# Kernel tuning notes

Measured on AMD Instinct MI355X. Metric: run time of the kernel, lower is better.

The kernel has to match this reference:

```python
import jax, jax.numpy as jnp
import numpy as np

EMB = 128
EA = 32
ET = 32
NN = 50000
NE = 320000
NBAND = 3
LAM = 0.01  # softshrink sparsity_threshold
LN_EPS = 1e-5


def _softshrink(x, lam=LAM):
    return jnp.where(x > lam, x - lam, jnp.where(x < -lam, x + lam, jnp.zeros_like(x)))


def _forward(hidden, edge_attr, edge_time_emb, boundary_condition,
             alpha, r1, i1, rb1, ib1, fre_w, fre_b,
             comb_w, comb_b, lin_w, lin_b, ln_g, ln_b, edge_index):
    num_nodes = hidden.shape[0]
    # gather source node features and concat edge features -> [E, d_in]
    x = jnp.concatenate([hidden[edge_index[0]], edge_attr, edge_time_emb], axis=1)
    # FreMLP: FFT over feature dim (real input -> complex64)
    x_fft = jnp.fft.fft(x)
    xr, xi = x_fft.real, x_fft.imag
    energy = jnp.sum(xr * xr + xi * xi, axis=-1)  # [E]
    energy_sum = jnp.sum(energy)
    outs = []
    for k in range(NBAND):
        factor = (2.0 * (k + 1) - 1.0) / (2.0 * NBAND)
        Qk = alpha[k] * factor * energy_sum
        bk = energy_sum / (alpha[k] * (2.0 * NBAND))
        mask = ((energy >= Qk - bk) & (energy <= Qk + bk)).astype(x.dtype)[:, None]
        fr = xr * mask
        fi = xi * mask
        # complex linear: (fr + i*fi) @ (r1 + i*i1) + (rb1 + i*ib1)
        o_r = fr @ r1[k] - fi @ i1[k] + rb1[k]
        o_i = fi @ r1[k] + fr @ i1[k] + ib1[k]
        o_r = _softshrink(jax.nn.relu(o_r))
        o_i = _softshrink(jax.nn.relu(o_i))
        outs.append(jax.lax.complex(o_r, o_i))
    y_fft = jnp.concatenate(outs, axis=-1)  # [E, NBAND*EMB] complex
    y = jnp.fft.ifft(y_fft).real
    msg = y @ fre_w + fre_b  # [E, EMB]
    # view_as_complex(msg, 0) -> view_as_real -> flatten: interleave real with zeros
    msg_ri = jnp.stack([msg, jnp.zeros_like(msg)], axis=-1).reshape(msg.shape[0], 2 * EMB)
    msg2 = msg_ri @ comb_w + comb_b  # [E, EMB]
    # scatter-reduce(sum) into destination nodes + boundary self-loops
    msg_aug = jnp.concatenate([msg2, boundary_condition], axis=0)
    idx_aug = jnp.concatenate([edge_index[1], jnp.arange(num_nodes, dtype=edge_index.dtype)])
    out = jax.ops.segment_sum(msg_aug, idx_aug, num_segments=num_nodes)
    out = out @ lin_w + lin_b
    mu = jnp.mean(out, axis=-1, keepdims=True)
    var = jnp.mean((out - mu) ** 2, axis=-1, keepdims=True)
    out = (out - mu) * jax.lax.rsqrt(var + LN_EPS) * ln_g + ln_b
    return jax.nn.relu(out)  # dropout is identity in eval mode


def setup_inputs() -> dict:
    key = jax.random.key(0)
    ks = jax.random.split(key, 16)
    d_in = EMB + EA + ET
    s = 0.02
    return {
        "hidden": jax.random.normal(ks[0], (NN, EMB), jnp.float32),
        "edge_attr": jax.random.normal(ks[1], (NE, EA), jnp.float32),
        "edge_time_emb": jax.random.normal(ks[2], (NE, ET), jnp.float32),
        "boundary_condition": jax.random.normal(ks[3], (NN, EMB), jnp.float32),
        "alpha": jnp.ones((NBAND,), jnp.float32),
        "r1": s * jax.random.normal(ks[4], (NBAND, d_in, EMB), jnp.float32),
        "i1": s * jax.random.normal(ks[5], (NBAND, d_in, EMB), jnp.float32),
        "rb1": s * jax.random.normal(ks[6], (NBAND, EMB), jnp.float32),
        "ib1": s * jax.random.normal(ks[7], (NBAND, EMB), jnp.float32),
        "fre_w": s * jax.random.normal(ks[8], (NBAND * EMB, EMB), jnp.float32),
        "fre_b": s * jax.random.normal(ks[9], (EMB,), jnp.float32),
        "comb_w": s * jax.random.normal(ks[10], (2 * EMB, EMB), jnp.float32),
        "comb_b": s * jax.random.normal(ks[11], (EMB,), jnp.float32),
        "lin_w": s * jax.random.normal(ks[12], (EMB, EMB), jnp.float32),
        "lin_b": s * jax.random.normal(ks[13], (EMB,), jnp.float32),
        "ln_g": jnp.ones((EMB,), jnp.float32),
        "ln_b": jnp.zeros((EMB,), jnp.float32),
        "edge_index": jax.random.randint(ks[14], (2, NE), 0, NN, dtype=jnp.int32),
    }


def reference(hidden, edge_attr, edge_time_emb, boundary_condition, alpha, r1, i1, rb1, ib1,
              fre_w, fre_b, comb_w, comb_b, lin_w, lin_b, ln_g, ln_b, edge_index):
    return _forward(hidden, edge_attr, edge_time_emb, boundary_condition, alpha, r1, i1,
                    rb1, ib1, fre_w, fre_b, comb_w, comb_b, lin_w, lin_b, ln_g, ln_b, edge_index)
```

## Files before the change

### kernel.cpp

```cpp
#include <hip/hip_runtime.h>
#include <hip/hip_bf16.h>

#define NNODES 50000
#define NEDGES 320000
#define EMB 128
#define DIN 192
#define NB 3
#define LAM 0.01f
#define LN_EPS 1e-5f
#define PI_F 3.14159265358979323846f

#define SCAN_B 196
#define SCAN_N (SCAN_B * 256)

typedef __attribute__((ext_vector_type(8))) short v8s;
typedef __attribute__((ext_vector_type(4))) float v4f;
typedef __attribute__((ext_vector_type(2))) float v2f;

#define WS_ESUM 0
#define WS_WB   16
#define WS_G2B  (WS_WB + 73728)
#define WS_G2   (WS_G2B + 49152)
#define WS_PHI  (WS_G2 + 98304)
#define WS_M    (WS_PHI + 98304)
#define WS_BB   (WS_M + 16384)
#define WS_GB2  (WS_BB + 768)
#define WS_CK   (WS_GB2 + 128)
#define WS_EN   (WS_CK + 384)
#define WS_NORM (WS_EN + NEDGES)
#define WS_CNT  (WS_NORM + NNODES)
#define WS_CUR  (WS_CNT + SCAN_N)
#define WS_PART (WS_CUR + SCAN_N)
#define WS_EIDS (WS_PART + 256)

__device__ __forceinline__ unsigned pk2(float a, float b) {
  __hip_bfloat162 h2 = __float22bfloat162_rn(make_float2(a, b));
  return *reinterpret_cast<unsigned*>(&h2);
}

__device__ __forceinline__ void atomic2(float* dp, float a, float b) {
#if __has_builtin(__builtin_amdgcn_flat_atomic_fadd_v2f32)
  v2f val; val.x = a; val.y = b;
  __builtin_amdgcn_flat_atomic_fadd_v2f32((v2f*)dp, val);
#else
  atomicAdd(dp, a); atomicAdd(dp + 1, b);
#endif
}

__global__ __launch_bounds__(256) void k_prep1(
    const float* __restrict__ r1, const float* __restrict__ i1,
    __hip_bfloat16* __restrict__ Wb, const float* __restrict__ comb_w,
    const float* __restrict__ lin_w, float* __restrict__ M,
    const float* __restrict__ fre_w, float* __restrict__ Phi,
    const float* __restrict__ hidden, float* __restrict__ norms) {
  __shared__ float cs[384], sn[384];
  const int t = threadIdx.x;
  const int b = blockIdx.x;
  if (b < 576) {
    if (t < 192) sincosf((2.f * PI_F / 192.f) * (float)t, &sn[t], &cs[t]);
    __syncthreads();
    int idx = b * 256 + t;
    int n = idx / 768, c = idx - (idx / 768) * 768;
    int k = c >> 8, col = c & 255;
    int isI = col >> 7, j = col & 127;
    const float* ap = (isI ? i1 : r1) + (size_t)k * DIN * EMB + j;
    const float* bp = (isI ? r1 : i1) + (size_t)k * DIN * EMB + j;
    float sgn = isI ? -1.f : 1.f;
    float acc = 0.f;
    int m = 0;
    for (int f = 0; f < DIN; ++f) {
      acc = fmaf(cs[m], ap[(size_t)f * EMB], fmaf(sgn * sn[m], bp[(size_t)f * EMB], acc));
      m += n; if (m >= 192) m -= 192;
    }
    int kc = n >> 5, quad = (n & 31) >> 3, jj = n & 7;
    int lane = quad * 16 + (col & 15);
    Wb[((((k * 6 + kc) * 16 + (col >> 4)) * 64) + lane) * 8 + jj] = __float2bfloat16(acc);
  } else if (b < 640) {
    int idx = (b - 576) * 256 + t;
    int j = idx >> 7, j2 = idx & 127;
    float acc = 0.f;
    for (int tt = 0; tt < 128; ++tt)
      acc = fmaf(comb_w[(2 * j) * 128 + tt], lin_w[tt * 128 + j2], acc);
    M[idx] = acc;
  } else if (b < 1024) {
    for (int i = t; i < 384; i += 256)
      sincosf((2.f * PI_F / 384.f) * (float)i, &sn[i], &cs[i]);
    __syncthreads();
    int idx = (b - 640) * 256 + t;
    int slot = idx >> 7, j1 = idx & 127;
    int k = slot >> 8, r = slot & 255;
    int isI = r >> 7;
    int f = k * 128 + (r & 127);
    const float* tp = isI ? sn : cs;
    float sg = isI ? -1.f : 1.f;
    float acc = 0.f;
    int m = 0;
    for (int n = 0; n < 384; ++n) {
      acc = fmaf(sg * tp[m], fre_w[n * 128 + j1], acc);
      m += f; if (m >= 384) m -= 384;
    }
    Phi[slot * 128 + j1] = acc * (1.f / 384.f);
  } else {
    const int w = t >> 6, lane = t & 63;
    const int n = (b - 1024) * 4 + w;
    const float2 v = ((const float2*)(hidden + (size_t)n * 128))[lane];
    float ss = v.x * v.x + v.y * v.y;
#pragma unroll
    for (int off = 32; off > 0; off >>= 1) ss += __shfl_xor(ss, off, 64);
    if (lane == 0) norms[n] = ss;
  }
}

__global__ __launch_bounds__(256) void k_prep2(
    const float* __restrict__ Phi, const float* __restrict__ M,
    float* __restrict__ G2, __hip_bfloat16* __restrict__ G2b,
    const float* __restrict__ norms, const float* __restrict__ eattr,
    const float* __restrict__ ett, const int* __restrict__ eidx,
    float* __restrict__ energies, float* __restrict__ esum,
    int* __restrict__ cnt) {
  const int t = threadIdx.x;
  const int b = blockIdx.x;
  if (b < 384) {
    int idx = b * 256 + t;
    int slot = idx >> 7, j2 = idx & 127;
    float acc = 0.f;
    for (int j1 = 0; j1 < 128; ++j1)
      acc = fmaf(Phi[slot * 128 + j1], M[j1 * 128 + j2], acc);
    G2[idx] = acc;
    int k = slot >> 8, s = slot & 255;
    int kc = s >> 5, quad = (s & 31) >> 3, jj = s & 7;
    G2b[((((k * 8 + kc) * 8 + (j2 >> 4)) * 64) + quad * 16 + (j2 & 15)) * 8 + jj] =
        __float2bfloat16(acc);
  } else {
    int e = (b - 384) * 256 + t;
    float ss = norms[eidx[e]];
    const float4* a4 = (const float4*)(eattr + (size_t)e * 32);
#pragma unroll
    for (int i = 0; i < 8; ++i) {
      float4 v = a4[i];
      ss += v.x * v.x + v.y * v.y + v.z * v.z + v.w * v.w;
    }
    const float4* t4 = (const float4*)(ett + (size_t)e * 32);
#pragma unroll
    for (int i = 0; i < 8; ++i) {
      float4 v = t4[i];
      ss += v.x * v.x + v.y * v.y + v.z * v.z + v.w * v.w;
    }
    float en = 192.f * ss;
    energies[e] = en;
    float tot = en;
#pragma unroll
    for (int off = 32; off > 0; off >>= 1) tot += __shfl_down(tot, off, 64);
    if ((t & 63) == 0) atomicAdd(esum, tot);
    atomicAdd(&cnt[eidx[NEDGES + e]], 1);
  }
}

__global__ __launch_bounds__(256) void k_prep3(
    const float* __restrict__ rb1, const float* __restrict__ ib1,
    const float* __restrict__ fre_b, const float* __restrict__ comb_b,
    const float* __restrict__ lin_w, const float* __restrict__ M,
    const float* __restrict__ G2, float* __restrict__ bb,
    float* __restrict__ gb2, float* __restrict__ ck,
    int* __restrict__ cnt, int* __restrict__ part) {
  __shared__ int sm[256];
  const int t = threadIdx.x;
  const int b = blockIdx.x;
  if (b < 5) {
    int idx = b * 256 + t;
    if (idx < 768) {
      int k = idx >> 8, r = idx & 255;
      bb[idx] = (r >= 128) ? ib1[k * 128 + (r & 127)] : rb1[k * 128 + r];
    } else if (idx < 896) {
      int j2 = idx - 768;
      float acc = 0.f;
      for (int j = 0; j < 128; ++j) acc += fre_b[j] * M[j * 128 + j2];
      for (int tt = 0; tt < 128; ++tt) acc += comb_b[tt] * lin_w[tt * 128 + j2];
      gb2[j2] = acc;
    } else if (idx < 1280) {
      int q = idx - 896;
      int k = q >> 7, j2 = q & 127;
      float acc = 0.f;
      for (int j = 0; j < 128; ++j) {
        float vr = rb1[k * 128 + j];
        vr = fmaxf(vr, 0.f); vr = (vr > LAM) ? vr - LAM : 0.f;
        float vi = ib1[k * 128 + j];
        vi = fmaxf(vi, 0.f); vi = (vi > LAM) ? vi - LAM : 0.f;
        acc += vr * G2[(k * 256 + j) * 128 + j2] + vi * G2[(k * 256 + 128 + j) * 128 + j2];
      }
      ck[k * 128 + j2] = acc;
    }
  } else {
    int blk = b - 5;
    int i = blk * 256 + t;
    int v = (i < NNODES) ? cnt[i] : 0;
    sm[t] = v;
    __syncthreads();
#pragma unroll
    for (int off = 1; off < 256; off <<= 1) {
      int x = (t >= off) ? sm[t - off] : 0;
      __syncthreads();
      sm[t] += x;
      __syncthreads();
    }
    cnt[i] = sm[t] - v;
    if (t == 255) part[blk] = sm[t];
  }
}

__global__ __launch_bounds__(256) void k_scanB(int* __restrict__ part) {
  __shared__ int sm[256];
  const int t = threadIdx.x;
  int v = (t < SCAN_B) ? part[t] : 0;
  sm[t] = v;
  __syncthreads();
#pragma unroll
  for (int off = 1; off < 256; off <<= 1) {
    int x = (t >= off) ? sm[t - off] : 0;
    __syncthreads();
    sm[t] += x;
    __syncthreads();
  }
  if (t < SCAN_B) part[t] = sm[t] - v;
}

__global__ __launch_bounds__(256) void k_scanC(const int* __restrict__ scanned,
                                               const int* __restrict__ part,
                                               int* __restrict__ cur) {
  int i = blockIdx.x * 256 + threadIdx.x;
  cur[i] = scanned[i] + part[blockIdx.x];
}

__global__ __launch_bounds__(256) void k_fill(const int* __restrict__ eidx,
                                              int* __restrict__ cur,
                                              int* __restrict__ eids) {
  int e = blockIdx.x * 256 + threadIdx.x;
  int pos = atomicAdd(&cur[eidx[NEDGES + e]], 1);
  eids[pos] = e;
}

#define XS_STR 200
#define OS_STR 264
#define ZS_STR 130
__global__ __launch_bounds__(512, 4) void k_edges(
    const float* __restrict__ hidden, const float* __restrict__ eattr,
    const float* __restrict__ ett, const float* __restrict__ alpha,
    const int* __restrict__ eidx, const int* __restrict__ eids,
    const __hip_bfloat16* __restrict__ Wb, const __hip_bfloat16* __restrict__ G2b,
    const float* __restrict__ bb, const float* __restrict__ gb2,
    const float* __restrict__ ck, const float* __restrict__ energies,
    const float* __restrict__ esum, float* __restrict__ accum) {
  __shared__ __align__(16) char smem[64 * XS_STR * 2 + 64 * OS_STR * 2];
  short* Xs = (short*)smem;
  short* Os = (short*)(smem + 64 * XS_STR * 2);
  float* Zs = (float*)smem;
  __shared__ float maskf[3][64];
  __shared__ int eid_s[64], srcs[64], dsts[64];
  __shared__ int tileact[3];

  const int t = threadIdx.x;
  const int e0 = blockIdx.x * 64;
  const int lane = t & 63, w = t >> 6;
  const int quad = lane >> 4, lc = lane & 15;

  if (t < 3) tileact[t] = 0;
  if (t < 64) {
    int eid = eids[e0 + t];
    eid_s[t] = eid;
    srcs[t] = eidx[eid];
    dsts[t] = eidx[NEDGES + eid];
    float en = energies[eid];
    float es = *esum;
#pragma unroll
    for (int k = 0; k < NB; ++k) {
      float a = alpha[k];
      float factor = (2.f * (k + 1) - 1.f) / (2.f * NB);
      float Q = a * factor * es;
      float b = es / (a * (2.f * NB));
      bool m = (en >= Q - b) && (en <= Q + b);
      maskf[k][t] = m ? 1.f : 0.f;
      if (m) atomicOr(&tileact[k], 1);
    }
  }
  __syncthreads();

#pragma unroll
  for (int it = 0; it < 4; ++it) {
    int i = t + it * 512;
    int e = i >> 5, c4 = i & 31;
    const float4 v = *(const float4*)(hidden + (size_t)srcs[e] * 128 + c4 * 4);
    unsigned* p = (unsigned*)&Xs[e * XS_STR + c4 * 4];
    p[0] = pk2(v.x, v.y); p[1] = pk2(v.z, v.w);
  }
#pragma unroll
  for (int it = 0; it < 2; ++it) {
    int i = t + it * 512;
    int e = i >> 4, q = i & 15;
    float4 v;
    if (q < 8) v = ((const float4*)(eattr + (size_t)eid_s[e] * 32))[q];
    else       v = ((const float4*)(ett + (size_t)eid_s[e] * 32))[q - 8];
    unsigned* p = (unsigned*)&Xs[e * XS_STR + 128 + q * 4];
    p[0] = pk2(v.x, v.y); p[1] = pk2(v.z, v.w);
  }
  __syncthreads();

  v4f acc2[4];
#pragma unroll
  for (int mt = 0; mt < 4; ++mt)
#pragma unroll
    for (int r = 0; r < 4; ++r) acc2[mt][r] = 0.f;

  for (int k = 0; k < NB; ++k) {
    if (!tileact[k]) continue;
    v4f accA[4][2];
#pragma unroll
    for (int mt = 0; mt < 4; ++mt)
#pragma unroll
      for (int n = 0; n < 2; ++n)
#pragma unroll
        for (int r = 0; r < 4; ++r) accA[mt][n][r] = 0.f;

#pragma unroll
    for (int kc = 0; kc < 6; ++kc) {
      v8s af[4];
#pragma unroll
      for (int mt = 0; mt < 4; ++mt)
        af[mt] = *(const v8s*)&Xs[(mt * 16 + lc) * XS_STR + kc * 32 + quad * 8];
      const __hip_bfloat16* wp = Wb + ((((k * 6 + kc) * 16 + 2 * w) * 64) + lane) * 8;
#pragma unroll
      for (int ntl = 0; ntl < 2; ++ntl) {
        v8s bfr = *(const v8s*)(const void*)(wp + ntl * 512);
#pragma unroll
        for (int mt = 0; mt < 4; ++mt)
          accA[mt][ntl] =
              __builtin_amdgcn_mfma_f32_16x16x32_bf16(af[mt], bfr, accA[mt][ntl], 0, 0, 0);
      }
    }
    __syncthreads();
#pragma unroll
    for (int mt = 0; mt < 4; ++mt)
#pragma unroll
      for (int ntl = 0; ntl < 2; ++ntl) {
        int col = w * 32 + ntl * 16 + lc;
        float bbv = bb[k * 256 + col];
#pragma unroll
        for (int reg = 0; reg < 4; ++reg) {
          int row = mt * 16 + quad * 4 + reg;
          float mk = maskf[k][row];
          float v = fmaf(mk, accA[mt][ntl][reg], bbv);
          v = fmaxf(v, 0.f);
          v = (v > LAM) ? v - LAM : 0.f;
          __hip_bfloat16 h = __float2bfloat16(v);
          Os[row * OS_STR + col] = *reinterpret_cast<short*>(&h);
        }
      }
    __syncthreads();
#pragma unroll
    for (int kc = 0; kc < 8; ++kc) {
      v8s of[4];
#pragma unroll
      for (int mt = 0; mt < 4; ++mt)
        of[mt] = *(const v8s*)&Os[(mt * 16 + lc) * OS_STR + kc * 32 + quad * 8];
      const __hip_bfloat16* gp = G2b + ((((k * 8 + kc) * 8 + w) * 64) + lane) * 8;
      v8s bfr = *(const v8s*)(const void*)gp;
#pragma unroll
      for (int mt = 0; mt < 4; ++mt)
        acc2[mt] = __builtin_amdgcn_mfma_f32_16x16x32_bf16(of[mt], bfr, acc2[mt], 0, 0, 0);
    }
  }

  __syncthreads();
  {
    int col = w * 16 + lc;
    float base = gb2[col];
#pragma unroll
    for (int k = 0; k < NB; ++k)
      if (!tileact[k]) base += ck[k * 128 + col];
#pragma unroll
    for (int mt = 0; mt < 4; ++mt)
#pragma unroll
      for (int reg = 0; reg < 4; ++reg) {
        int row = mt * 16 + quad * 4 + reg;
        Zs[row * ZS_STR + col] = acc2[mt][reg] + base;
      }
  }
  __syncthreads();
  if (w < 2) {
    int c = 2 * lane;
    int r0 = w * 32;
    float s0 = 0.f, s1 = 0.f;
#pragma unroll
    for (int r = 0; r < 32; ++r) {
      int row = r0 + r;
      s0 += Zs[row * ZS_STR + c];
      s1 += Zs[row * ZS_STR + c + 1];
      int d = dsts[row];
      if (r == 31 || dsts[row + 1] != d) {
        atomic2(accum + (size_t)d * 128 + c, s0, s1);
        s0 = 0.f; s1 = 0.f;
      }
    }
  }
}

__global__ __launch_bounds__(256) void k_nodes(const float* __restrict__ boundary,
                                               const float* __restrict__ lin_w,
                                               const float* __restrict__ lin_b,
                                               const float* __restrict__ ln_g,
                                               const float* __restrict__ ln_b,
                                               float* __restrict__ out) {
  __shared__ float lw[32][128];
  const int t = threadIdx.x;
  const int w = t >> 6, lane = t & 63;
  const int n = blockIdx.x * 4 + w;
  float a0 = out[(size_t)n * 128 + lane] + lin_b[lane];
  float a1 = out[(size_t)n * 128 + 64 + lane] + lin_b[64 + lane];
  for (int cb = 0; cb < 128; cb += 32) {
    __syncthreads();
#pragma unroll
    for (int it = 0; it < 16; ++it) {
      int i = t + it * 256;
      lw[i >> 7][i & 127] = lin_w[(cb + (i >> 7)) * 128 + (i & 127)];
    }
    __syncthreads();
#pragma unroll
    for (int r = 0; r < 32; ++r) {
      float bv = boundary[(size_t)n * 128 + cb + r];
      a0 = fmaf(bv, lw[r][lane], a0);
      a1 = fmaf(bv, lw[r][64 + lane], a1);
    }
  }
  float s = a0 + a1, sq = a0 * a0 + a1 * a1;
#pragma unroll
  for (int off = 32; off > 0; off >>= 1) {
    s += __shfl_xor(s, off, 64);
    sq += __shfl_xor(sq, off, 64);
  }
  float mu = s * (1.f / 128.f);
  float var = sq * (1.f / 128.f) - mu * mu;
  float rs = 1.f / sqrtf(var + LN_EPS);
  float y0 = (a0 - mu) * rs * ln_g[lane] + ln_b[lane];
  float y1 = (a1 - mu) * rs * ln_g[64 + lane] + ln_b[64 + lane];
  out[(size_t)n * 128 + lane] = fmaxf(y0, 0.f);
  out[(size_t)n * 128 + 64 + lane] = fmaxf(y1, 0.f);
}

extern "C" void kernel_launch(void* const* d_in, const int* in_sizes, int n_in,
                              void* d_out, int out_size, void* d_ws, size_t ws_size,
                              hipStream_t stream) {
  const float* hidden   = (const float*)d_in[0];
  const float* eattr    = (const float*)d_in[1];
  const float* ett      = (const float*)d_in[2];
  const float* boundary = (const float*)d_in[3];
  const float* alpha    = (const float*)d_in[4];
  const float* r1       = (const float*)d_in[5];
  const float* i1       = (const float*)d_in[6];
  const float* rb1      = (const float*)d_in[7];
  const float* ib1      = (const float*)d_in[8];
  const float* fre_w    = (const float*)d_in[9];
  const float* fre_b    = (const float*)d_in[10];
  const float* comb_w   = (const float*)d_in[11];
  const float* comb_b   = (const float*)d_in[12];
  const float* lin_w    = (const float*)d_in[13];
  const float* lin_b    = (const float*)d_in[14];
  const float* ln_g     = (const float*)d_in[15];
  const float* ln_b     = (const float*)d_in[16];
  const int*   eidx     = (const int*)d_in[17];
  float* ws  = (float*)d_ws;
  float* out = (float*)d_out;
  __hip_bfloat16* Wb  = (__hip_bfloat16*)(ws + WS_WB);
  __hip_bfloat16* G2b = (__hip_bfloat16*)(ws + WS_G2B);
  int* cnt  = (int*)(ws + WS_CNT);
  int* cur  = (int*)(ws + WS_CUR);
  int* part = (int*)(ws + WS_PART);
  int* eids = (int*)(ws + WS_EIDS);

  hipMemsetAsync(ws + WS_ESUM, 0, 16 * sizeof(float), stream);
  hipMemsetAsync(cnt, 0, SCAN_N * sizeof(int), stream);
  hipMemsetAsync(out, 0, (size_t)NNODES * EMB * sizeof(float), stream);

  k_prep1<<<1024 + 12500, 256, 0, stream>>>(r1, i1, Wb, comb_w, lin_w, ws + WS_M,
                                            fre_w, ws + WS_PHI, hidden, ws + WS_NORM);
  k_prep2<<<384 + NEDGES / 256, 256, 0, stream>>>(ws + WS_PHI, ws + WS_M, ws + WS_G2,
                                                  G2b, ws + WS_NORM, eattr, ett, eidx,
                                                  ws + WS_EN, ws + WS_ESUM, cnt);
  k_prep3<<<5 + SCAN_B, 256, 0, stream>>>(rb1, ib1, fre_b, comb_b, lin_w, ws + WS_M,
                                          ws + WS_G2, ws + WS_BB, ws + WS_GB2,
                                          ws + WS_CK, cnt, part);
  k_scanB<<<1, 256, 0, stream>>>(part);
  k_scanC<<<SCAN_B, 256, 0, stream>>>(cnt, part, cur);
  k_fill<<<NEDGES / 256, 256, 0, stream>>>(eidx, cur, eids);
  k_edges<<<NEDGES / 64, 512, 0, stream>>>(hidden, eattr, ett, alpha, eidx, eids,
                                           Wb, G2b, ws + WS_BB, ws + WS_GB2,
                                           ws + WS_CK, ws + WS_EN, ws + WS_ESUM, out);
  k_nodes<<<NNODES / 4, 256, 0, stream>>>(boundary, lin_w, lin_b, ln_g, ln_b, out);
}
```

Before: 556.1 us.

## Make edge kernel persistent with double-buffered gather and fold memsets into prep

The edge kernel becomes persistent with 500 blocks, each looping over 10 tiles. It double-buffers the per-tile metadata in LDS and prefetches the next tile's gathered features into registers while the current tile runs its MFMA work, aiming to hide gather latency. The three memsets move into extra blocks of the first prep kernel, and the two-pass scan fix-up is merged into one kernel that reduces the partial sums per block, cutting launch count. The trade-offs are fewer resident blocks, more register pressure from the prefetch buffers, and the grid no longer overlapping tiles across many blocks.

```diff
diff --git a/kernel.cpp b/kernel.cpp
--- a/kernel.cpp
+++ b/kernel.cpp
@@ -12,6 +12,10 @@
 
 #define SCAN_B 196
 #define SCAN_N (SCAN_B * 256)
+
+#define TILES (NEDGES / 64)
+#define EGRID 500
+#define EITER (TILES / EGRID)
 
 typedef __attribute__((ext_vector_type(8))) short v8s;
 typedef __attribute__((ext_vector_type(4))) float v4f;
@@ -47,12 +51,19 @@
 #endif
 }
 
+__device__ __forceinline__ void bar_lds() {
+  asm volatile("s_waitcnt lgkmcnt(0)" ::: "memory");
+  __builtin_amdgcn_s_barrier();
+  asm volatile("" ::: "memory");
+}
+
 __global__ __launch_bounds__(256) void k_prep1(
     const float* __restrict__ r1, const float* __restrict__ i1,
     __hip_bfloat16* __restrict__ Wb, const float* __restrict__ comb_w,
     const float* __restrict__ lin_w, float* __restrict__ M,
     const float* __restrict__ fre_w, float* __restrict__ Phi,
-    const float* __restrict__ hidden, float* __restrict__ norms) {
+    const float* __restrict__ hidden, float* __restrict__ norms,
+    float* __restrict__ outz, int* __restrict__ cnt, float* __restrict__ esum) {
   __shared__ float cs[384], sn[384];
   const int t = threadIdx.x;
   const int b = blockIdx.x;
@@ -100,7 +111,7 @@
       m += f; if (m >= 384) m -= 384;
     }
     Phi[slot * 128 + j1] = acc * (1.f / 384.f);
-  } else {
+  } else if (b < 13524) {
     const int w = t >> 6, lane = t & 63;
     const int n = (b - 1024) * 4 + w;
     const float2 v = ((const float2*)(hidden + (size_t)n * 128))[lane];
@@ -108,6 +119,12 @@
 #pragma unroll
     for (int off = 32; off > 0; off >>= 1) ss += __shfl_xor(ss, off, 64);
     if (lane == 0) norms[n] = ss;
+    float2 z; z.x = 0.f; z.y = 0.f;
+    ((float2*)(outz + (size_t)n * 128))[lane] = z;
+  } else if (b < 13720) {
+    cnt[(b - 13524) * 256 + t] = 0;
+  } else {
+    if (t < 16) esum[t] = 0.f;
   }
 }
 
@@ -208,27 +225,20 @@
   }
 }
 
-__global__ __launch_bounds__(256) void k_scanB(int* __restrict__ part) {
+__global__ __launch_bounds__(256) void k_scan(const int* __restrict__ cnt,
+                                              const int* __restrict__ part,
+                                              int* __restrict__ cur) {
   __shared__ int sm[256];
   const int t = threadIdx.x;
-  int v = (t < SCAN_B) ? part[t] : 0;
-  sm[t] = v;
+  const int b = blockIdx.x;
+  sm[t] = (t < b) ? part[t] : 0;
   __syncthreads();
 #pragma unroll
-  for (int off = 1; off < 256; off <<= 1) {
-    int x = (t >= off) ? sm[t - off] : 0;
+  for (int off = 128; off > 0; off >>= 1) {
+    if (t < off) sm[t] += sm[t + off];
     __syncthreads();
-    sm[t] += x;
-    __syncthreads();
-  }
-  if (t < SCAN_B) part[t] = sm[t] - v;
-}
-
-__global__ __launch_bounds__(256) void k_scanC(const int* __restrict__ scanned,
-                                               const int* __restrict__ part,
-                                               int* __restrict__ cur) {
-  int i = blockIdx.x * 256 + threadIdx.x;
-  cur[i] = scanned[i] + part[blockIdx.x];
+  }
+  cur[b * 256 + t] = cnt[b * 256 + t] + sm[0];
 }
 
 __global__ __launch_bounds__(256) void k_fill(const int* __restrict__ eidx,
@@ -242,6 +252,55 @@
 #define XS_STR 200
 #define OS_STR 264
 #define ZS_STR 130
+
+#define LOADM_PUBLISH(B)                                                       \
+  do {                                                                         \
+    if (t < 3) tileact[B][t] = 0;                                              \
+    if (t < 64) {                                                              \
+      eid_s[B][t] = eidA;                                                      \
+      srcs[B][t] = srcA;                                                       \
+      dsts[B][t] = dstA;                                                       \
+      _Pragma("unroll") for (int k = 0; k < NB; ++k) {                         \
+        bool m_ = (enA >= lo[k]) && (enA <= hi[k]);                            \
+        maskf[B][k][t] = m_ ? 1.f : 0.f;                                       \
+        if (m_) atomicOr(&tileact[B][k], 1);                                   \
+      }                                                                        \
+    }                                                                          \
+  } while (0)
+
+#define GATHER(B)                                                              \
+  do {                                                                         \
+    _Pragma("unroll") for (int it = 0; it < 4; ++it) {                         \
+      int i = t + it * 512;                                                    \
+      hreg[it] = *(const float4*)(hidden + (size_t)srcs[B][i >> 5] * 128 +     \
+                                  (i & 31) * 4);                               \
+    }                                                                          \
+    _Pragma("unroll") for (int it = 0; it < 2; ++it) {                         \
+      int i = t + it * 512;                                                    \
+      int e = i >> 4, q = i & 15;                                              \
+      float4 v_;                                                               \
+      if (q < 8) v_ = ((const float4*)(eattr + (size_t)eid_s[B][e] * 32))[q];  \
+      else       v_ = ((const float4*)(ett + (size_t)eid_s[B][e] * 32))[q - 8];\
+      areg[it] = v_;                                                           \
+    }                                                                          \
+  } while (0)
+
+#define WRITEX()                                                               \
+  do {                                                                         \
+    _Pragma("unroll") for (int it = 0; it < 4; ++it) {                         \
+      int i = t + it * 512;                                                    \
+      unsigned* p = (unsigned*)&Xs[(i >> 5) * XS_STR + (i & 31) * 4];          \
+      p[0] = pk2(hreg[it].x, hreg[it].y);                                      \
+      p[1] = pk2(hreg[it].z, hreg[it].w);                                      \
+    }                                                                          \
+    _Pragma("unroll") for (int it = 0; it < 2; ++it) {                         \
+      int i = t + it * 512;                                                    \
+      unsigned* p = (unsigned*)&Xs[(i >> 4) * XS_STR + 128 + (i & 15) * 4];    \
+      p[0] = pk2(areg[it].x, areg[it].y);                                      \
+      p[1] = pk2(areg[it].z, areg[it].w);                                      \
+    }                                                                          \
+  } while (0)
+
 __global__ __launch_bounds__(512, 4) void k_edges(
     const float* __restrict__ hidden, const float* __restrict__ eattr,
     const float* __restrict__ ett, const float* __restrict__ alpha,
@@ -254,152 +313,161 @@
   short* Xs = (short*)smem;
   short* Os = (short*)(smem + 64 * XS_STR * 2);
   float* Zs = (float*)smem;
-  __shared__ float maskf[3][64];
-  __shared__ int eid_s[64], srcs[64], dsts[64];
-  __shared__ int tileact[3];
+  __shared__ float maskf[2][3][64];
+  __shared__ int eid_s[2][64], srcs[2][64], dsts[2][64];
+  __shared__ int tileact[2][3];
 
   const int t = threadIdx.x;
-  const int e0 = blockIdx.x * 64;
   const int lane = t & 63, w = t >> 6;
   const int quad = lane >> 4, lc = lane & 15;
-
-  if (t < 3) tileact[t] = 0;
-  if (t < 64) {
-    int eid = eids[e0 + t];
-    eid_s[t] = eid;
-    srcs[t] = eidx[eid];
-    dsts[t] = eidx[NEDGES + eid];
-    float en = energies[eid];
-    float es = *esum;
+  const int tile = blockIdx.x;
+
+  float lo[NB], hi[NB];
+  {
+    const float es = *esum;
 #pragma unroll
     for (int k = 0; k < NB; ++k) {
       float a = alpha[k];
       float factor = (2.f * (k + 1) - 1.f) / (2.f * NB);
       float Q = a * factor * es;
-      float b = es / (a * (2.f * NB));
-      bool m = (en >= Q - b) && (en <= Q + b);
-      maskf[k][t] = m ? 1.f : 0.f;
-      if (m) atomicOr(&tileact[k], 1);
-    }
-  }
-  __syncthreads();
-
-#pragma unroll
-  for (int it = 0; it < 4; ++it) {
-    int i = t + it * 512;
-    int e = i >> 5, c4 = i & 31;
-    const float4 v = *(const float4*)(hidden + (size_t)srcs[e] * 128 + c4 * 4);
-    unsigned* p = (unsigned*)&Xs[e * XS_STR + c4 * 4];
-    p[0] = pk2(v.x, v.y); p[1] = pk2(v.z, v.w);
-  }
-#pragma unroll
-  for (int it = 0; it < 2; ++it) {
-    int i = t + it * 512;
-    int e = i >> 4, q = i & 15;
-    float4 v;
-    if (q < 8) v = ((const float4*)(eattr + (size_t)eid_s[e] * 32))[q];
-    else       v = ((const float4*)(ett + (size_t)eid_s[e] * 32))[q - 8];
-    unsigned* p = (unsigned*)&Xs[e * XS_STR + 128 + q * 4];
-    p[0] = pk2(v.x, v.y); p[1] = pk2(v.z, v.w);
-  }
-  __syncthreads();
-
-  v4f acc2[4];
-#pragma unroll
-  for (int mt = 0; mt < 4; ++mt)
-#pragma unroll
-    for (int r = 0; r < 4; ++r) acc2[mt][r] = 0.f;
-
-  for (int k = 0; k < NB; ++k) {
-    if (!tileact[k]) continue;
-    v4f accA[4][2];
+      float bw = es / (a * (2.f * NB));
+      lo[k] = Q - bw;
+      hi[k] = Q + bw;
+    }
+  }
+
+  float4 hreg[4], areg[2];
+  int eidA = 0, srcA = 0, dstA = 0, eidB = 0;
+  float enA = 0.f;
+
+  if (t < 64) {
+    int e_ = eids[tile * 64 + t];
+    eidA = e_; srcA = eidx[e_]; dstA = eidx[NEDGES + e_]; enA = energies[e_];
+  }
+  LOADM_PUBLISH(0);
+  if (t < 64) {
+    int e_ = eids[(tile + EGRID) * 64 + t];
+    eidA = e_; srcA = eidx[e_]; dstA = eidx[NEDGES + e_]; enA = energies[e_];
+    eidB = eids[(tile + 2 * EGRID) * 64 + t];
+  }
+  bar_lds();
+  GATHER(0);
+
+#pragma unroll 1
+  for (int ti = 0; ti < EITER; ++ti) {
+    const int cb = ti & 1;
+    WRITEX();
+    if (ti + 1 < EITER) LOADM_PUBLISH(cb ^ 1);
+    if (t < 64) {
+      if (ti + 2 < EITER) {
+        eidA = eidB;
+        srcA = eidx[eidB]; dstA = eidx[NEDGES + eidB]; enA = energies[eidB];
+      }
+      if (ti + 3 < EITER)
+        eidB = eids[(tile + (ti + 3) * EGRID) * 64 + t];
+    }
+    bar_lds();
+
+    v4f acc2[4];
 #pragma unroll
     for (int mt = 0; mt < 4; ++mt)
 #pragma unroll
-      for (int n = 0; n < 2; ++n)
-#pragma unroll
-        for (int r = 0; r < 4; ++r) accA[mt][n][r] = 0.f;
-
-#pragma unroll
-    for (int kc = 0; kc < 6; ++kc) {
-      v8s af[4];
+      for (int r = 0; r < 4; ++r) acc2[mt][r] = 0.f;
+
+    for (int k = 0; k < NB; ++k) {
+      if (!tileact[cb][k]) continue;
+      v4f accA[4][2];
 #pragma unroll
       for (int mt = 0; mt < 4; ++mt)
-        af[mt] = *(const v8s*)&Xs[(mt * 16 + lc) * XS_STR + kc * 32 + quad * 8];
-      const __hip_bfloat16* wp = Wb + ((((k * 6 + kc) * 16 + 2 * w) * 64) + lane) * 8;
-#pragma unroll
-      for (int ntl = 0; ntl < 2; ++ntl) {
-        v8s bfr = *(const v8s*)(const void*)(wp + ntl * 512);
+#pragma unroll
+        for (int n = 0; n < 2; ++n)
+#pragma unroll
+          for (int r = 0; r < 4; ++r) accA[mt][n][r] = 0.f;
+
+#pragma unroll
+      for (int kc = 0; kc < 6; ++kc) {
+        v8s af[4];
 #pragma unroll
         for (int mt = 0; mt < 4; ++mt)
-          accA[mt][ntl] =
-              __builtin_amdgcn_mfma_f32_16x16x32_bf16(af[mt], bfr, accA[mt][ntl], 0, 0, 0);
+          af[mt] = *(const v8s*)&Xs[(mt * 16 + lc) * XS_STR + kc * 32 + quad * 8];
+        const __hip_bfloat16* wp = Wb + ((((k * 6 + kc) * 16 + 2 * w) * 64) + lane) * 8;
+#pragma unroll
+        for (int ntl = 0; ntl < 2; ++ntl) {
+          v8s bfr = *(const v8s*)(const void*)(wp + ntl * 512);
+#pragma unroll
+          for (int mt = 0; mt < 4; ++mt)
+            accA[mt][ntl] =
+                __builtin_amdgcn_mfma_f32_16x16x32_bf16(af[mt], bfr, accA[mt][ntl], 0, 0, 0);
+        }
       }
-    }
-    __syncthreads();
-#pragma unroll
-    for (int mt = 0; mt < 4; ++mt)
-#pragma unroll
-      for (int ntl = 0; ntl < 2; ++ntl) {
-        int col = w * 32 + ntl * 16 + lc;
-        float bbv = bb[k * 256 + col];
+      bar_lds();
+#pragma unroll
+      for (int mt = 0; mt < 4; ++mt)
+#pragma unroll
+        for (int ntl = 0; ntl < 2; ++ntl) {
+          int col = w * 32 + ntl * 16 + lc;
+          float bbv = bb[k * 256 + col];
+#pragma unroll
+          for (int reg = 0; reg < 4; ++reg) {
+            int row = mt * 16 + quad * 4 + reg;
+            float mk = maskf[cb][k][row];
+            float v = fmaf(mk, accA[mt][ntl][reg], bbv);
+            v = fmaxf(v, 0.f);
+            v = (v > LAM) ? v - LAM : 0.f;
+            __hip_bfloat16 h = __float2bfloat16(v);
+            Os[row * OS_STR + col] = *reinterpret_cast<short*>(&h);
+          }
+        }
+      bar_lds();
+#pragma unroll
+      for (int kc = 0; kc < 8; ++kc) {
+        v8s of[4];
+#pragma unroll
+        for (int mt = 0; mt < 4; ++mt)
+          of[mt] = *(const v8s*)&Os[(mt * 16 + lc) * OS_STR + kc * 32 + quad * 8];
+        const __hip_bfloat16* gp = G2b + ((((k * 8 + kc) * 8 + w) * 64) + lane) * 8;
+        v8s bfr = *(const v8s*)(const void*)gp;
+#pragma unroll
+        for (int mt = 0; mt < 4; ++mt)
+          acc2[mt] = __builtin_amdgcn_mfma_f32_16x16x32_bf16(of[mt], bfr, acc2[mt], 0, 0, 0);
+      }
+    }
+
+    if (ti + 1 < EITER) GATHER(cb ^ 1);
+
+    bar_lds();
+    {
+      int col = w * 16 + lc;
+      float base = gb2[col];
+#pragma unroll
+      for (int k = 0; k < NB; ++k)
+        if (!tileact[cb][k]) base += ck[k * 128 + col];
+#pragma unroll
+      for (int mt = 0; mt < 4; ++mt)
 #pragma unroll
         for (int reg = 0; reg < 4; ++reg) {
           int row = mt * 16 + quad * 4 + reg;
-          float mk = maskf[k][row];
-          float v = fmaf(mk, accA[mt][ntl][reg], bbv);
-          v = fmaxf(v, 0.f);
-          v = (v > LAM) ? v - LAM : 0.f;
-          __hip_bfloat16 h = __float2bfloat16(v);
-          Os[row * OS_STR + col] = *reinterpret_cast<short*>(&h);
+          Zs[row * ZS_STR + col] = acc2[mt][reg] + base;
+        }
+    }
+    bar_lds();
+    if (w < 2) {
+      int c = 2 * lane;
+      int r0 = w * 32;
+      float s0 = 0.f, s1 = 0.f;
+#pragma unroll
+      for (int r = 0; r < 32; ++r) {
+        int row = r0 + r;
+        s0 += Zs[row * ZS_STR + c];
+        s1 += Zs[row * ZS_STR + c + 1];
+        int d = dsts[cb][row];
+        if (r == 31 || dsts[cb][row + 1] != d) {
+          atomic2(accum + (size_t)d * 128 + c, s0, s1);
+          s0 = 0.f; s1 = 0.f;
         }
       }
-    __syncthreads();
-#pragma unroll
-    for (int kc = 0; kc < 8; ++kc) {
-      v8s of[4];
-#pragma unroll
-      for (int mt = 0; mt < 4; ++mt)
-        of[mt] = *(const v8s*)&Os[(mt * 16 + lc) * OS_STR + kc * 32 + quad * 8];
-      const __hip_bfloat16* gp = G2b + ((((k * 8 + kc) * 8 + w) * 64) + lane) * 8;
-      v8s bfr = *(const v8s*)(const void*)gp;
-#pragma unroll
-      for (int mt = 0; mt < 4; ++mt)
-        acc2[mt] = __builtin_amdgcn_mfma_f32_16x16x32_bf16(of[mt], bfr, acc2[mt], 0, 0, 0);
-    }
-  }
-
-  __syncthreads();
-  {
-    int col = w * 16 + lc;
-    float base = gb2[col];
-#pragma unroll
-    for (int k = 0; k < NB; ++k)
-      if (!tileact[k]) base += ck[k * 128 + col];
-#pragma unroll
-    for (int mt = 0; mt < 4; ++mt)
-#pragma unroll
-      for (int reg = 0; reg < 4; ++reg) {
-        int row = mt * 16 + quad * 4 + reg;
-        Zs[row * ZS_STR + col] = acc2[mt][reg] + base;
-      }
-  }
-  __syncthreads();
-  if (w < 2) {
-    int c = 2 * lane;
-    int r0 = w * 32;
-    float s0 = 0.f, s1 = 0.f;
-#pragma unroll
-    for (int r = 0; r < 32; ++r) {
-      int row = r0 + r;
-      s0 += Zs[row * ZS_STR + c];
-      s1 += Zs[row * ZS_STR + c + 1];
-      int d = dsts[row];
-      if (r == 31 || dsts[row + 1] != d) {
-        atomic2(accum + (size_t)d * 128 + c, s0, s1);
-        s0 = 0.f; s1 = 0.f;
-      }
-    }
+    }
+    if (ti + 1 < EITER) bar_lds();
   }
 }
 
@@ -475,23 +543,19 @@
   int* part = (int*)(ws + WS_PART);
   int* eids = (int*)(ws + WS_EIDS);
 
-  hipMemsetAsync(ws + WS_ESUM, 0, 16 * sizeof(float), stream);
-  hipMemsetAsync(cnt, 0, SCAN_N * sizeof(int), stream);
-  hipMemsetAsync(out, 0, (size_t)NNODES * EMB * sizeof(float), stream);
-
-  k_prep1<<<1024 + 12500, 256, 0, stream>>>(r1, i1, Wb, comb_w, lin_w, ws + WS_M,
-                                            fre_w, ws + WS_PHI, hidden, ws + WS_NORM);
+  k_prep1<<<13721, 256, 0, stream>>>(r1, i1, Wb, comb_w, lin_w, ws + WS_M,
+                                     fre_w, ws + WS_PHI, hidden, ws + WS_NORM,
+                                     out, cnt, ws + WS_ESUM);
   k_prep2<<<384 + NEDGES / 256, 256, 0, stream>>>(ws + WS_PHI, ws + WS_M, ws + WS_G2,
                                                   G2b, ws + WS_NORM, eattr, ett, eidx,
                                                   ws + WS_EN, ws + WS_ESUM, cnt);
   k_prep3<<<5 + SCAN_B, 256, 0, stream>>>(rb1, ib1, fre_b, comb_b, lin_w, ws + WS_M,
                                           ws + WS_G2, ws + WS_BB, ws + WS_GB2,
                                           ws + WS_CK, cnt, part);
-  k_scanB<<<1, 256, 0, stream>>>(part);
-  k_scanC<<<SCAN_B, 256, 0, stream>>>(cnt, part, cur);
+  k_scan<<<SCAN_B, 256, 0, stream>>>(cnt, part, cur);
   k_fill<<<NEDGES / 256, 256, 0, stream>>>(eidx, cur, eids);
-  k_edges<<<NEDGES / 64, 512, 0, stream>>>(hidden, eattr, ett, alpha, eidx, eids,
-                                           Wb, G2b, ws + WS_BB, ws + WS_GB2,
-                                           ws + WS_CK, ws + WS_EN, ws + WS_ESUM, out);
+  k_edges<<<EGRID, 512, 0, stream>>>(hidden, eattr, ett, alpha, eidx, eids,
+                                     Wb, G2b, ws + WS_BB, ws + WS_GB2,
+                                     ws + WS_CK, ws + WS_EN, ws + WS_ESUM, out);
   k_nodes<<<NNODES / 4, 256, 0, stream>>>(boundary, lin_w, lin_b, ln_g, ln_b, out);
 }
```

Measured after the change: 620.6 us. 11.6% more time.
